# Kernel optimization log

Hardware: AMD Instinct MI355X
Metric: run time of the kernel (lower is better)

## Reference

```python
import jax, jax.numpy as jnp
import numpy as np

NEG = -9e15
EPS = 1e-5

def setup_inputs() -> dict:
    key = jax.random.key(0)
    k1, k2, k3, k4 = jax.random.split(key, 4)
    B, S, D = 4, 2048, 1024
    q = jax.random.normal(k1, (B, S, D), dtype=jnp.float32)
    k = jax.random.normal(k2, (B, S, D), dtype=jnp.float32)
    v = jax.random.normal(k3, (B, S, D), dtype=jnp.float32)
    mask = jax.random.randint(k4, (B, S, S), 0, 2, dtype=jnp.int32)
    gamma = jnp.ones((D,), dtype=jnp.float32)
    beta = jnp.zeros((D,), dtype=jnp.float32)
    return {"q": q, "k": k, "v": v, "mask": mask, "gamma": gamma, "beta": beta}

def reference(q, k, v, mask, gamma, beta):
    d_k = q.shape[-1]
    # scaled dot-product attention: [B,S,S] logits materialized as in original
    logits = jnp.einsum('bsd,btd->bst', q, k) / jnp.sqrt(jnp.asarray(d_k, q.dtype))
    logits = jnp.where(mask == 0, jnp.asarray(NEG, logits.dtype), logits)
    attn = jax.nn.softmax(logits, axis=-1)
    x = jnp.einsum('bst,btd->bsd', attn, v)
    # dropout is identity at inference; LayerNorm over last dim
    mu = jnp.mean(x, axis=-1, keepdims=True)
    var = jnp.mean(jnp.square(x - mu), axis=-1, keepdims=True)
    xhat = (x - mu) * jax.lax.rsqrt(var + EPS)
    return xhat * gamma + beta
```

## Files before the change

### kernel.cpp

```cpp
#include <hip/hip_runtime.h>
#include <hip/hip_bf16.h>

typedef unsigned short u16;
typedef __attribute__((ext_vector_type(8))) short bf16x8;
typedef __attribute__((ext_vector_type(4))) float f32x4;
typedef __attribute__((ext_vector_type(4))) float float4v;
typedef __attribute__((ext_vector_type(4))) short short4v;

#define BB 4
#define SS 2048
#define DD 1024
#define SCALE 0.03125f

__device__ __forceinline__ u16 f2bf(float x){
    unsigned u = __float_as_uint(x);
    return (u16)((u + 0x7fffu + ((u >> 16) & 1u)) >> 16);
}

#define GLD16(g, l) __builtin_amdgcn_global_load_lds( \
    (const __attribute__((address_space(1))) unsigned int*)(g), \
    (__attribute__((address_space(3))) unsigned int*)(l), 16, 0, 0)

__global__ void conv_bf16_kernel(const float* __restrict__ in,
                                 u16* __restrict__ out, int n4){
    int i = blockIdx.x * 256 + threadIdx.x;
    if (i >= n4) return;
    float4v v = ((const float4v*)in)[i];
    short4v o;
    o[0] = (short)f2bf(v[0]); o[1] = (short)f2bf(v[1]);
    o[2] = (short)f2bf(v[2]); o[3] = (short)f2bf(v[3]);
    ((short4v*)out)[i] = o;
}

__global__ void transpose_v_kernel(const float* __restrict__ v,
                                   u16* __restrict__ vt){
    __shared__ float tile[64][65];
    const int b  = blockIdx.z;
    const int s0 = blockIdx.x << 6;
    const int d0 = blockIdx.y << 6;
    const int tx = threadIdx.x & 15;
    const int ty = threadIdx.x >> 4;
#pragma unroll
    for (int kk = 0; kk < 4; ++kk){
        const float* p = v + ((b * SS + s0 + ty + 16 * kk) * DD) + d0 + tx * 4;
        float4v val = *(const float4v*)p;
        tile[ty + 16 * kk][tx * 4 + 0] = val[0];
        tile[ty + 16 * kk][tx * 4 + 1] = val[1];
        tile[ty + 16 * kk][tx * 4 + 2] = val[2];
        tile[ty + 16 * kk][tx * 4 + 3] = val[3];
    }
    __syncthreads();
#pragma unroll
    for (int kk = 0; kk < 4; ++kk){
        int dy = ty + 16 * kk;
        short4v o;
        o[0] = (short)f2bf(tile[tx * 4 + 0][dy]);
        o[1] = (short)f2bf(tile[tx * 4 + 1][dy]);
        o[2] = (short)f2bf(tile[tx * 4 + 2][dy]);
        o[3] = (short)f2bf(tile[tx * 4 + 3][dy]);
        *(short4v*)&vt[((b * DD + d0 + dy) * SS) + s0 + tx * 4] = o;
    }
}

__global__ void zero_f32(float* __restrict__ p, int n){
    int i = blockIdx.x * 256 + threadIdx.x;
    if (i < n) p[i] = 0.f;
}

__global__ __launch_bounds__(256, 3) void qk_kernel(
    const u16* __restrict__ Qb, const u16* __restrict__ Kb,
    const int* __restrict__ mask, u16* __restrict__ P,
    float* __restrict__ rowsum)
{
    __shared__ __align__(16) u16 Abuf[128 * 32];
    __shared__ __align__(16) u16 Bbuf[128 * 32];
    __shared__ float rsred[2][128];

    const int tid  = threadIdx.x;
    const int wid  = tid >> 6, lane = tid & 63;
    const int l16  = lane & 15, g4 = lane >> 4;
    const int wr   = wid >> 1,  wc = wid & 1;
    const int b    = blockIdx.z;
    const int row0 = blockIdx.x << 7;
    const int col0 = blockIdx.y << 7;

    f32x4 acc[4][4];
    const f32x4 z4 = {0.f, 0.f, 0.f, 0.f};
#pragma unroll
    for (int i = 0; i < 4; ++i)
#pragma unroll
        for (int j = 0; j < 4; ++j) acc[i][j] = z4;

    const int off0 = wid * 1024 + lane * 16;
    const int ar0  = off0 >> 6;
    const int ac0  = (off0 & 63) >> 1;

    const u16* gQ = Qb + ((size_t)(b * SS + row0 + ar0)) * DD + ac0;
    const u16* gK = Kb + ((size_t)(b * SS + col0 + ar0)) * DD + ac0;

    for (int kk = 0; kk < DD; kk += 32){
        GLD16(gQ + kk,           (char*)Abuf + wid * 1024);
        GLD16(gQ + 64 * DD + kk, (char*)Abuf + 4096 + wid * 1024);
        GLD16(gK + kk,           (char*)Bbuf + wid * 1024);
        GLD16(gK + 64 * DD + kk, (char*)Bbuf + 4096 + wid * 1024);
        __syncthreads();
        bf16x8 af[4], bfr[4];
#pragma unroll
        for (int i = 0; i < 4; ++i){
            af[i]  = *(const bf16x8*)&Abuf[(wr * 64 + i * 16 + l16) * 32 + g4 * 8];
            bfr[i] = *(const bf16x8*)&Bbuf[(wc * 64 + i * 16 + l16) * 32 + g4 * 8];
        }
#pragma unroll
        for (int i = 0; i < 4; ++i)
#pragma unroll
            for (int j = 0; j < 4; ++j)
                acc[i][j] = __builtin_amdgcn_mfma_f32_16x16x32_bf16(af[i], bfr[j], acc[i][j], 0, 0, 0);
        __syncthreads();
    }

    float rs[4][4];
#pragma unroll
    for (int i = 0; i < 4; ++i)
#pragma unroll
        for (int r = 0; r < 4; ++r) rs[i][r] = 0.f;

#pragma unroll
    for (int i = 0; i < 4; ++i){
#pragma unroll
        for (int j = 0; j < 4; ++j){
#pragma unroll
            for (int r = 0; r < 4; ++r){
                const int grow = row0 + wr * 64 + i * 16 + g4 * 4 + r;
                const int gcol = col0 + wc * 64 + j * 16 + l16;
                const size_t idx = ((size_t)(b * SS + grow)) * SS + gcol;
                int m = mask[idx];
                float e = m ? __expf(acc[i][j][r] * SCALE) : 0.f;
                P[idx] = f2bf(e);
                rs[i][r] += e;
            }
        }
    }
#pragma unroll
    for (int i = 0; i < 4; ++i)
#pragma unroll
        for (int r = 0; r < 4; ++r){
            float v = rs[i][r];
            v += __shfl_xor(v, 1); v += __shfl_xor(v, 2);
            v += __shfl_xor(v, 4); v += __shfl_xor(v, 8);
            if (l16 == 0) rsred[wc][wr * 64 + i * 16 + g4 * 4 + r] = v;
        }
    __syncthreads();
    if (tid < 128)
        atomicAdd(&rowsum[b * SS + row0 + tid], rsred[0][tid] + rsred[1][tid]);
}

__global__ __launch_bounds__(256, 3) void pv_kernel(
    const u16* __restrict__ P, const u16* __restrict__ Vt,
    const float* __restrict__ rowsum, u16* __restrict__ Xn)
{
    __shared__ __align__(16) u16 Abuf[128 * 32];
    __shared__ __align__(16) u16 Bbuf[128 * 32];

    const int tid  = threadIdx.x;
    const int wid  = tid >> 6, lane = tid & 63;
    const int l16  = lane & 15, g4 = lane >> 4;
    const int wr   = wid >> 1,  wc = wid & 1;
    const int b    = blockIdx.z;
    const int row0 = blockIdx.x << 7;
    const int col0 = blockIdx.y << 7;

    f32x4 acc[4][4];
    const f32x4 z4 = {0.f, 0.f, 0.f, 0.f};
#pragma unroll
    for (int i = 0; i < 4; ++i)
#pragma unroll
        for (int j = 0; j < 4; ++j) acc[i][j] = z4;

    const int off0 = wid * 1024 + lane * 16;
    const int ar0  = off0 >> 6;
    const int ac0  = (off0 & 63) >> 1;

    const u16* gP = P  + ((size_t)(b * SS + row0 + ar0)) * SS + ac0;
    const u16* gV = Vt + ((size_t)(b * DD + col0 + ar0)) * SS + ac0;

    for (int kk = 0; kk < SS; kk += 32){
        GLD16(gP + kk,           (char*)Abuf + wid * 1024);
        GLD16(gP + 64 * SS + kk, (char*)Abuf + 4096 + wid * 1024);
        GLD16(gV + kk,           (char*)Bbuf + wid * 1024);
        GLD16(gV + 64 * SS + kk, (char*)Bbuf + 4096 + wid * 1024);
        __syncthreads();
        bf16x8 af[4], bfr[4];
#pragma unroll
        for (int i = 0; i < 4; ++i){
            af[i]  = *(const bf16x8*)&Abuf[(wr * 64 + i * 16 + l16) * 32 + g4 * 8];
            bfr[i] = *(const bf16x8*)&Bbuf[(wc * 64 + i * 16 + l16) * 32 + g4 * 8];
        }
#pragma unroll
        for (int i = 0; i < 4; ++i)
#pragma unroll
            for (int j = 0; j < 4; ++j)
                acc[i][j] = __builtin_amdgcn_mfma_f32_16x16x32_bf16(af[i], bfr[j], acc[i][j], 0, 0, 0);
        __syncthreads();
    }

#pragma unroll
    for (int i = 0; i < 4; ++i){
        float inv[4];
#pragma unroll
        for (int r = 0; r < 4; ++r)
            inv[r] = 1.f / rowsum[b * SS + row0 + wr * 64 + i * 16 + g4 * 4 + r];
#pragma unroll
        for (int j = 0; j < 4; ++j){
#pragma unroll
            for (int r = 0; r < 4; ++r){
                const int grow = row0 + wr * 64 + i * 16 + g4 * 4 + r;
                const int gcol = col0 + wc * 64 + j * 16 + l16;
                Xn[((size_t)(b * SS + grow)) * DD + gcol] = f2bf(acc[i][j][r] * inv[r]);
            }
        }
    }
}

__global__ __launch_bounds__(256) void ln_kernel(
    const u16* __restrict__ Xn, const float* __restrict__ gamma,
    const float* __restrict__ beta, float* __restrict__ out)
{
    __shared__ float red[2][4];
    const int row = blockIdx.x;
    const int t = threadIdx.x;
    short4v xv = *(const short4v*)&Xn[(size_t)row * DD + t * 4];
    float x[4];
#pragma unroll
    for (int j = 0; j < 4; ++j)
        x[j] = __uint_as_float(((unsigned)(u16)xv[j]) << 16);
    float s  = x[0] + x[1] + x[2] + x[3];
    float sq = x[0]*x[0] + x[1]*x[1] + x[2]*x[2] + x[3]*x[3];
#pragma unroll
    for (int d = 1; d < 64; d <<= 1){ s += __shfl_xor(s, d); sq += __shfl_xor(sq, d); }
    const int wv = t >> 6;
    if ((t & 63) == 0){ red[0][wv] = s; red[1][wv] = sq; }
    __syncthreads();
    float S  = red[0][0] + red[0][1] + red[0][2] + red[0][3];
    float Sq = red[1][0] + red[1][1] + red[1][2] + red[1][3];
    float mu = S * (1.f / 1024.f);
    float var = Sq * (1.f / 1024.f) - mu * mu;
    float rstd = rsqrtf(var + 1e-5f);
    float4v g  = *(const float4v*)&gamma[t * 4];
    float4v be = *(const float4v*)&beta[t * 4];
    float4v o;
#pragma unroll
    for (int j = 0; j < 4; ++j) o[j] = (x[j] - mu) * rstd * g[j] + be[j];
    *(float4v*)&out[(size_t)row * DD + t * 4] = o;
}

extern "C" void kernel_launch(void* const* d_in, const int* in_sizes, int n_in,
                              void* d_out, int out_size, void* d_ws, size_t ws_size,
                              hipStream_t stream) {
    const float* q     = (const float*)d_in[0];
    const float* k     = (const float*)d_in[1];
    const float* v     = (const float*)d_in[2];
    const int*   mask  = (const int*)d_in[3];
    const float* gamma = (const float*)d_in[4];
    const float* beta  = (const float*)d_in[5];
    float* out = (float*)d_out;

    u16* Qb = (u16*)d_ws;
    u16* Kb = Qb + (size_t)BB * SS * DD;
    u16* Vt = Kb + (size_t)BB * SS * DD;
    u16* P  = Vt + (size_t)BB * SS * DD;
    u16* Xn = P  + (size_t)BB * SS * SS;
    float* rowsum = (float*)(Xn + (size_t)BB * SS * DD);

    const int n4 = BB * SS * DD / 4;
    conv_bf16_kernel<<<n4 / 256, 256, 0, stream>>>(q, Qb, n4);
    conv_bf16_kernel<<<n4 / 256, 256, 0, stream>>>(k, Kb, n4);
    transpose_v_kernel<<<dim3(SS / 64, DD / 64, BB), 256, 0, stream>>>(v, Vt);
    zero_f32<<<BB * SS / 256, 256, 0, stream>>>(rowsum, BB * SS);

    qk_kernel<<<dim3(16, 16, BB), 256, 0, stream>>>(Qb, Kb, mask, P, rowsum);
    pv_kernel<<<dim3(16, 8, BB), 256, 0, stream>>>(P, Vt, rowsum, Xn);
    ln_kernel<<<BB * SS, 256, 0, stream>>>(Xn, gamma, beta, out);
}
```

Baseline: 162.9 us.

## Double-buffer LDS tiles in QK and PV GEMMs, swizzle block order, fold scale into Q

Both GEMM kernels now use two LDS buffers, so the global-to-LDS load of the next K-tile is issued before the MFMA work on the current tile, with one barrier per iteration instead of two. The 3D grid becomes a flat grid with an XCD-aware swizzle that groups neighbouring tiles on the same die for better L2 reuse, and the launch-bounds occupancy hint rises from 3 to 4. The 1/sqrt(d) scale moves into the Q bf16 conversion, removing a multiply from the exp epilogue. The risks are higher LDS use per block and a possible shift in bf16 rounding because the scale is now applied before conversion.

```diff
diff --git a/kernel.cpp b/kernel.cpp
--- a/kernel.cpp
+++ b/kernel.cpp
@@ -10,7 +10,6 @@
 #define BB 4
 #define SS 2048
 #define DD 1024
-#define SCALE 0.03125f
 
 __device__ __forceinline__ u16 f2bf(float x){
     unsigned u = __float_as_uint(x);
@@ -22,13 +21,13 @@
     (__attribute__((address_space(3))) unsigned int*)(l), 16, 0, 0)
 
 __global__ void conv_bf16_kernel(const float* __restrict__ in,
-                                 u16* __restrict__ out, int n4){
+                                 u16* __restrict__ out, int n4, float scale){
     int i = blockIdx.x * 256 + threadIdx.x;
     if (i >= n4) return;
     float4v v = ((const float4v*)in)[i];
     short4v o;
-    o[0] = (short)f2bf(v[0]); o[1] = (short)f2bf(v[1]);
-    o[2] = (short)f2bf(v[2]); o[3] = (short)f2bf(v[3]);
+    o[0] = (short)f2bf(v[0] * scale); o[1] = (short)f2bf(v[1] * scale);
+    o[2] = (short)f2bf(v[2] * scale); o[3] = (short)f2bf(v[3] * scale);
     ((short4v*)out)[i] = o;
 }
 
@@ -67,22 +66,25 @@
     if (i < n) p[i] = 0.f;
 }
 
-__global__ __launch_bounds__(256, 3) void qk_kernel(
+__global__ __launch_bounds__(256, 4) void qk_kernel(
     const u16* __restrict__ Qb, const u16* __restrict__ Kb,
     const int* __restrict__ mask, u16* __restrict__ P,
     float* __restrict__ rowsum)
 {
-    __shared__ __align__(16) u16 Abuf[128 * 32];
-    __shared__ __align__(16) u16 Bbuf[128 * 32];
+    __shared__ __align__(16) u16 Abuf[2][128 * 32];
+    __shared__ __align__(16) u16 Bbuf[2][128 * 32];
     __shared__ float rsred[2][128];
+
+    const int flat = blockIdx.x;
+    const int swz  = (flat & 7) * 128 + (flat >> 3);
+    const int bx = swz & 15, by = (swz >> 4) & 15, b = swz >> 8;
 
     const int tid  = threadIdx.x;
     const int wid  = tid >> 6, lane = tid & 63;
     const int l16  = lane & 15, g4 = lane >> 4;
     const int wr   = wid >> 1,  wc = wid & 1;
-    const int b    = blockIdx.z;
-    const int row0 = blockIdx.x << 7;
-    const int col0 = blockIdx.y << 7;
+    const int row0 = bx << 7;
+    const int col0 = by << 7;
 
     f32x4 acc[4][4];
     const f32x4 z4 = {0.f, 0.f, 0.f, 0.f};
@@ -94,21 +96,29 @@
     const int off0 = wid * 1024 + lane * 16;
     const int ar0  = off0 >> 6;
     const int ac0  = (off0 & 63) >> 1;
+    const int ldso = wid * 1024 + lane * 16;
 
     const u16* gQ = Qb + ((size_t)(b * SS + row0 + ar0)) * DD + ac0;
     const u16* gK = Kb + ((size_t)(b * SS + col0 + ar0)) * DD + ac0;
 
-    for (int kk = 0; kk < DD; kk += 32){
-        GLD16(gQ + kk,           (char*)Abuf + wid * 1024);
-        GLD16(gQ + 64 * DD + kk, (char*)Abuf + 4096 + wid * 1024);
-        GLD16(gK + kk,           (char*)Bbuf + wid * 1024);
-        GLD16(gK + 64 * DD + kk, (char*)Bbuf + 4096 + wid * 1024);
-        __syncthreads();
+#define QK_STAGE(t, bi) { \
+    GLD16(gQ + (t) * 32,            (char*)Abuf[bi] + ldso); \
+    GLD16(gQ + 64 * DD + (t) * 32,  (char*)Abuf[bi] + 4096 + ldso); \
+    GLD16(gK + (t) * 32,            (char*)Bbuf[bi] + ldso); \
+    GLD16(gK + 64 * DD + (t) * 32,  (char*)Bbuf[bi] + 4096 + ldso); }
+
+    QK_STAGE(0, 0);
+    __syncthreads();
+
+    const int NT = DD / 32;
+    for (int t = 0; t < NT; ++t){
+        const int cur = t & 1;
+        if (t + 1 < NT) QK_STAGE(t + 1, cur ^ 1);
         bf16x8 af[4], bfr[4];
 #pragma unroll
         for (int i = 0; i < 4; ++i){
-            af[i]  = *(const bf16x8*)&Abuf[(wr * 64 + i * 16 + l16) * 32 + g4 * 8];
-            bfr[i] = *(const bf16x8*)&Bbuf[(wc * 64 + i * 16 + l16) * 32 + g4 * 8];
+            af[i]  = *(const bf16x8*)&Abuf[cur][(wr * 64 + i * 16 + l16) * 32 + g4 * 8];
+            bfr[i] = *(const bf16x8*)&Bbuf[cur][(wc * 64 + i * 16 + l16) * 32 + g4 * 8];
         }
 #pragma unroll
         for (int i = 0; i < 4; ++i)
@@ -117,6 +127,7 @@
                 acc[i][j] = __builtin_amdgcn_mfma_f32_16x16x32_bf16(af[i], bfr[j], acc[i][j], 0, 0, 0);
         __syncthreads();
     }
+#undef QK_STAGE
 
     float rs[4][4];
 #pragma unroll
@@ -134,7 +145,7 @@
                 const int gcol = col0 + wc * 64 + j * 16 + l16;
                 const size_t idx = ((size_t)(b * SS + grow)) * SS + gcol;
                 int m = mask[idx];
-                float e = m ? __expf(acc[i][j][r] * SCALE) : 0.f;
+                float e = m ? __expf(acc[i][j][r]) : 0.f;
                 P[idx] = f2bf(e);
                 rs[i][r] += e;
             }
@@ -154,20 +165,23 @@
         atomicAdd(&rowsum[b * SS + row0 + tid], rsred[0][tid] + rsred[1][tid]);
 }
 
-__global__ __launch_bounds__(256, 3) void pv_kernel(
+__global__ __launch_bounds__(256, 4) void pv_kernel(
     const u16* __restrict__ P, const u16* __restrict__ Vt,
     const float* __restrict__ rowsum, u16* __restrict__ Xn)
 {
-    __shared__ __align__(16) u16 Abuf[128 * 32];
-    __shared__ __align__(16) u16 Bbuf[128 * 32];
+    __shared__ __align__(16) u16 Abuf[2][128 * 32];
+    __shared__ __align__(16) u16 Bbuf[2][128 * 32];
+
+    const int flat = blockIdx.x;
+    const int swz  = (flat & 7) * 64 + (flat >> 3);
+    const int bx = swz & 15, by = (swz >> 4) & 7, b = swz >> 7;
 
     const int tid  = threadIdx.x;
     const int wid  = tid >> 6, lane = tid & 63;
     const int l16  = lane & 15, g4 = lane >> 4;
     const int wr   = wid >> 1,  wc = wid & 1;
-    const int b    = blockIdx.z;
-    const int row0 = blockIdx.x << 7;
-    const int col0 = blockIdx.y << 7;
+    const int row0 = bx << 7;
+    const int col0 = by << 7;
 
     f32x4 acc[4][4];
     const f32x4 z4 = {0.f, 0.f, 0.f, 0.f};
@@ -179,21 +193,29 @@
     const int off0 = wid * 1024 + lane * 16;
     const int ar0  = off0 >> 6;
     const int ac0  = (off0 & 63) >> 1;
+    const int ldso = wid * 1024 + lane * 16;
 
     const u16* gP = P  + ((size_t)(b * SS + row0 + ar0)) * SS + ac0;
     const u16* gV = Vt + ((size_t)(b * DD + col0 + ar0)) * SS + ac0;
 
-    for (int kk = 0; kk < SS; kk += 32){
-        GLD16(gP + kk,           (char*)Abuf + wid * 1024);
-        GLD16(gP + 64 * SS + kk, (char*)Abuf + 4096 + wid * 1024);
-        GLD16(gV + kk,           (char*)Bbuf + wid * 1024);
-        GLD16(gV + 64 * SS + kk, (char*)Bbuf + 4096 + wid * 1024);
-        __syncthreads();
+#define PV_STAGE(t, bi) { \
+    GLD16(gP + (t) * 32,            (char*)Abuf[bi] + ldso); \
+    GLD16(gP + 64 * SS + (t) * 32,  (char*)Abuf[bi] + 4096 + ldso); \
+    GLD16(gV + (t) * 32,            (char*)Bbuf[bi] + ldso); \
+    GLD16(gV + 64 * SS + (t) * 32,  (char*)Bbuf[bi] + 4096 + ldso); }
+
+    PV_STAGE(0, 0);
+    __syncthreads();
+
+    const int NT = SS / 32;
+    for (int t = 0; t < NT; ++t){
+        const int cur = t & 1;
+        if (t + 1 < NT) PV_STAGE(t + 1, cur ^ 1);
         bf16x8 af[4], bfr[4];
 #pragma unroll
         for (int i = 0; i < 4; ++i){
-            af[i]  = *(const bf16x8*)&Abuf[(wr * 64 + i * 16 + l16) * 32 + g4 * 8];
-            bfr[i] = *(const bf16x8*)&Bbuf[(wc * 64 + i * 16 + l16) * 32 + g4 * 8];
+            af[i]  = *(const bf16x8*)&Abuf[cur][(wr * 64 + i * 16 + l16) * 32 + g4 * 8];
+            bfr[i] = *(const bf16x8*)&Bbuf[cur][(wc * 64 + i * 16 + l16) * 32 + g4 * 8];
         }
 #pragma unroll
         for (int i = 0; i < 4; ++i)
@@ -202,6 +224,7 @@
                 acc[i][j] = __builtin_amdgcn_mfma_f32_16x16x32_bf16(af[i], bfr[j], acc[i][j], 0, 0, 0);
         __syncthreads();
     }
+#undef PV_STAGE
 
 #pragma unroll
     for (int i = 0; i < 4; ++i){
@@ -272,12 +295,12 @@
     float* rowsum = (float*)(Xn + (size_t)BB * SS * DD);
 
     const int n4 = BB * SS * DD / 4;
-    conv_bf16_kernel<<<n4 / 256, 256, 0, stream>>>(q, Qb, n4);
-    conv_bf16_kernel<<<n4 / 256, 256, 0, stream>>>(k, Kb, n4);
+    conv_bf16_kernel<<<n4 / 256, 256, 0, stream>>>(q, Qb, n4, 0.03125f);
+    conv_bf16_kernel<<<n4 / 256, 256, 0, stream>>>(k, Kb, n4, 1.0f);
     transpose_v_kernel<<<dim3(SS / 64, DD / 64, BB), 256, 0, stream>>>(v, Vt);
     zero_f32<<<BB * SS / 256, 256, 0, stream>>>(rowsum, BB * SS);
 
-    qk_kernel<<<dim3(16, 16, BB), 256, 0, stream>>>(Qb, Kb, mask, P, rowsum);
-    pv_kernel<<<dim3(16, 8, BB), 256, 0, stream>>>(P, Vt, rowsum, Xn);
+    qk_kernel<<<BB * 16 * 16, 256, 0, stream>>>(Qb, Kb, mask, P, rowsum);
+    pv_kernel<<<BB * 16 * 8, 256, 0, stream>>>(P, Vt, rowsum, Xn);
     ln_kernel<<<BB * SS, 256, 0, stream>>>(Xn, gamma, beta, out);
 }
```

New measurement: 162.7 us. No clear change (-0.2%).

## Rewrite QK and PV GEMMs with larger swizzled tiles and double-buffered pipelining

Applied to the files above, without the earlier changes.

Both matmul kernels move to 512-thread blocks with larger tiles (256x256 for QK, 128x256 for PV) and a BK of 64. Global-to-LDS loads are double-buffered with explicit vmcnt waits, and MFMA phases are wrapped in s_setprio and sched barriers. LDS reads use an XOR-swizzled layout to avoid bank conflicts, and the grid is a 1D launch remapped for locality. The 1/sqrt(d) scale is folded into the Q bf16 conversion, and row sums are now accumulated with per-wave atomics. This costs more LDS and registers per block, lowering occupancy, and adds more atomic traffic on the row sums.

```diff
diff --git a/kernel.cpp b/kernel.cpp
--- a/kernel.cpp
+++ b/kernel.cpp
@@ -10,7 +10,6 @@
 #define BB 4
 #define SS 2048
 #define DD 1024
-#define SCALE 0.03125f
 
 __device__ __forceinline__ u16 f2bf(float x){
     unsigned u = __float_as_uint(x);
@@ -21,14 +20,18 @@
     (const __attribute__((address_space(1))) unsigned int*)(g), \
     (__attribute__((address_space(3))) unsigned int*)(l), 16, 0, 0)
 
+#define SCHED0() __builtin_amdgcn_sched_barrier(0)
+#define PH_PRE()  SCHED0(); __builtin_amdgcn_s_barrier(); SCHED0(); __builtin_amdgcn_s_setprio(1)
+#define PH_POST() __builtin_amdgcn_s_setprio(0); SCHED0(); __builtin_amdgcn_s_barrier(); SCHED0()
+
 __global__ void conv_bf16_kernel(const float* __restrict__ in,
-                                 u16* __restrict__ out, int n4){
+                                 u16* __restrict__ out, int n4, float scale){
     int i = blockIdx.x * 256 + threadIdx.x;
     if (i >= n4) return;
     float4v v = ((const float4v*)in)[i];
     short4v o;
-    o[0] = (short)f2bf(v[0]); o[1] = (short)f2bf(v[1]);
-    o[2] = (short)f2bf(v[2]); o[3] = (short)f2bf(v[3]);
+    o[0] = (short)f2bf(v[0] * scale); o[1] = (short)f2bf(v[1] * scale);
+    o[2] = (short)f2bf(v[2] * scale); o[3] = (short)f2bf(v[3] * scale);
     ((short4v*)out)[i] = o;
 }
 
@@ -67,107 +70,175 @@
     if (i < n) p[i] = 0.f;
 }
 
-__global__ __launch_bounds__(256, 3) void qk_kernel(
+__global__ __launch_bounds__(512, 2) void qk_kernel(
     const u16* __restrict__ Qb, const u16* __restrict__ Kb,
     const int* __restrict__ mask, u16* __restrict__ P,
     float* __restrict__ rowsum)
 {
-    __shared__ __align__(16) u16 Abuf[128 * 32];
-    __shared__ __align__(16) u16 Bbuf[128 * 32];
-    __shared__ float rsred[2][128];
-
-    const int tid  = threadIdx.x;
-    const int wid  = tid >> 6, lane = tid & 63;
-    const int l16  = lane & 15, g4 = lane >> 4;
-    const int wr   = wid >> 1,  wc = wid & 1;
-    const int b    = blockIdx.z;
-    const int row0 = blockIdx.x << 7;
-    const int col0 = blockIdx.y << 7;
-
-    f32x4 acc[4][4];
+    __shared__ __align__(16) u16 As[2][256 * 64];
+    __shared__ __align__(16) u16 Bs[2][256 * 64];
+
+    const int swz = ((blockIdx.x & 7) << 5) + (blockIdx.x >> 3);
+    const int b   = swz >> 6;
+    const int bx  = (swz >> 3) & 7;
+    const int by  = swz & 7;
+    const int row0 = bx << 8, col0 = by << 8;
+
+    const int tid = threadIdx.x;
+    const int wid = tid >> 6, lane = tid & 63;
+    const int l16 = lane & 15, g4 = lane >> 4;
+    const int wr = wid >> 2, wc = wid & 3;
+
+    const int sr   = tid >> 3;
+    const int scol = ((tid & 7) ^ (sr & 7)) << 3;
+    const u16* gA = Qb + (size_t)(b * SS + row0 + sr) * DD + scol;
+    const u16* gB = Kb + (size_t)(b * SS + col0 + sr) * DD + scol;
+    char* const lA0 = (char*)As[0] + tid * 16;
+    char* const lB0 = (char*)Bs[0] + tid * 16;
+    char* const lA1 = (char*)As[1] + tid * 16;
+    char* const lB1 = (char*)Bs[1] + tid * 16;
+
+    const int aRow = (wr * 128 + l16) << 7;
+    const int bRow = (wc * 64  + l16) << 7;
+    const int cx0  = (g4 << 4) ^ ((l16 & 7) << 4);
+
+    f32x4 acc[8][4];
     const f32x4 z4 = {0.f, 0.f, 0.f, 0.f};
 #pragma unroll
-    for (int i = 0; i < 4; ++i)
+    for (int i = 0; i < 8; ++i)
 #pragma unroll
         for (int j = 0; j < 4; ++j) acc[i][j] = z4;
 
-    const int off0 = wid * 1024 + lane * 16;
-    const int ar0  = off0 >> 6;
-    const int ac0  = (off0 & 63) >> 1;
-
-    const u16* gQ = Qb + ((size_t)(b * SS + row0 + ar0)) * DD + ac0;
-    const u16* gK = Kb + ((size_t)(b * SS + col0 + ar0)) * DD + ac0;
-
-    for (int kk = 0; kk < DD; kk += 32){
-        GLD16(gQ + kk,           (char*)Abuf + wid * 1024);
-        GLD16(gQ + 64 * DD + kk, (char*)Abuf + 4096 + wid * 1024);
-        GLD16(gK + kk,           (char*)Bbuf + wid * 1024);
-        GLD16(gK + 64 * DD + kk, (char*)Bbuf + 4096 + wid * 1024);
-        __syncthreads();
-        bf16x8 af[4], bfr[4];
-#pragma unroll
-        for (int i = 0; i < 4; ++i){
-            af[i]  = *(const bf16x8*)&Abuf[(wr * 64 + i * 16 + l16) * 32 + g4 * 8];
-            bfr[i] = *(const bf16x8*)&Bbuf[(wc * 64 + i * 16 + l16) * 32 + g4 * 8];
-        }
-#pragma unroll
-        for (int i = 0; i < 4; ++i)
-#pragma unroll
-            for (int j = 0; j < 4; ++j)
-                acc[i][j] = __builtin_amdgcn_mfma_f32_16x16x32_bf16(af[i], bfr[j], acc[i][j], 0, 0, 0);
-        __syncthreads();
-    }
-
-    float rs[4][4];
-#pragma unroll
-    for (int i = 0; i < 4; ++i)
-#pragma unroll
-        for (int r = 0; r < 4; ++r) rs[i][r] = 0.f;
-
-#pragma unroll
-    for (int i = 0; i < 4; ++i){
-#pragma unroll
-        for (int j = 0; j < 4; ++j){
+#define STAGE_QK(kt, la, lb) { \
+    const u16* ga_ = gA + (kt) * 64; \
+    const u16* gb_ = gB + (kt) * 64; \
+    GLD16(ga_,            (la)); \
+    GLD16(ga_ +  64 * DD, (la) + 8192); \
+    GLD16(ga_ + 128 * DD, (la) + 16384); \
+    GLD16(ga_ + 192 * DD, (la) + 24576); \
+    GLD16(gb_,            (lb)); \
+    GLD16(gb_ +  64 * DD, (lb) + 8192); \
+    GLD16(gb_ + 128 * DD, (lb) + 16384); \
+    GLD16(gb_ + 192 * DD, (lb) + 24576); }
+
+#define LDA4(Ab_, mh, kx) { \
+    const char* p_ = (const char*)(Ab_) + aRow + (mh) * 8192 + ((kx) ? (cx0 ^ 64) : cx0); \
+    fa0 = *(const bf16x8*)(p_); \
+    fa1 = *(const bf16x8*)(p_ + 2048); \
+    fa2 = *(const bf16x8*)(p_ + 4096); \
+    fa3 = *(const bf16x8*)(p_ + 6144); }
+
+#define LDB4(Bb_, kx) { \
+    const char* p_ = (const char*)(Bb_) + bRow + ((kx) ? (cx0 ^ 64) : cx0); \
+    fb0 = *(const bf16x8*)(p_); \
+    fb1 = *(const bf16x8*)(p_ + 2048); \
+    fb2 = *(const bf16x8*)(p_ + 4096); \
+    fb3 = *(const bf16x8*)(p_ + 6144); }
+
+#define MROWQ(mi, fa) \
+    acc[mi][0] = __builtin_amdgcn_mfma_f32_16x16x32_bf16(fa, fb0, acc[mi][0],0,0,0); \
+    acc[mi][1] = __builtin_amdgcn_mfma_f32_16x16x32_bf16(fa, fb1, acc[mi][1],0,0,0); \
+    acc[mi][2] = __builtin_amdgcn_mfma_f32_16x16x32_bf16(fa, fb2, acc[mi][2],0,0,0); \
+    acc[mi][3] = __builtin_amdgcn_mfma_f32_16x16x32_bf16(fa, fb3, acc[mi][3],0,0,0);
+
+    STAGE_QK(0, lA0, lB0);
+    STAGE_QK(1, lA1, lB1);
+    asm volatile("s_waitcnt vmcnt(8)" ::: "memory");
+    SCHED0(); __builtin_amdgcn_s_barrier(); SCHED0();
+
+#pragma unroll 1
+    for (int it = 0; it < 8; ++it){
+        bf16x8 fa0, fa1, fa2, fa3, fb0, fb1, fb2, fb3;
+        LDA4(As[0], 0, 0); LDB4(Bs[0], 0);
+        PH_PRE(); MROWQ(0,fa0) MROWQ(1,fa1) MROWQ(2,fa2) MROWQ(3,fa3) PH_POST();
+        LDA4(As[0], 1, 0);
+        PH_PRE(); MROWQ(4,fa0) MROWQ(5,fa1) MROWQ(6,fa2) MROWQ(7,fa3) PH_POST();
+        LDA4(As[0], 0, 1); LDB4(Bs[0], 1);
+        PH_PRE(); MROWQ(0,fa0) MROWQ(1,fa1) MROWQ(2,fa2) MROWQ(3,fa3) PH_POST();
+        LDA4(As[0], 1, 1);
+        PH_PRE(); MROWQ(4,fa0) MROWQ(5,fa1) MROWQ(6,fa2) MROWQ(7,fa3) PH_POST();
+        if (it < 7){
+            STAGE_QK(2*it+2, lA0, lB0);
+            asm volatile("s_waitcnt vmcnt(8)" ::: "memory");
+        } else {
+            asm volatile("s_waitcnt vmcnt(0)" ::: "memory");
+        }
+        SCHED0(); __builtin_amdgcn_s_barrier(); SCHED0();
+        LDA4(As[1], 0, 0); LDB4(Bs[1], 0);
+        PH_PRE(); MROWQ(0,fa0) MROWQ(1,fa1) MROWQ(2,fa2) MROWQ(3,fa3) PH_POST();
+        LDA4(As[1], 1, 0);
+        PH_PRE(); MROWQ(4,fa0) MROWQ(5,fa1) MROWQ(6,fa2) MROWQ(7,fa3) PH_POST();
+        LDA4(As[1], 0, 1); LDB4(Bs[1], 1);
+        PH_PRE(); MROWQ(0,fa0) MROWQ(1,fa1) MROWQ(2,fa2) MROWQ(3,fa3) PH_POST();
+        LDA4(As[1], 1, 1);
+        PH_PRE(); MROWQ(4,fa0) MROWQ(5,fa1) MROWQ(6,fa2) MROWQ(7,fa3) PH_POST();
+        if (it < 7){
+            STAGE_QK(2*it+3, lA1, lB1);
+            asm volatile("s_waitcnt vmcnt(8)" ::: "memory");
+            SCHED0(); __builtin_amdgcn_s_barrier(); SCHED0();
+        }
+    }
+#undef STAGE_QK
+#undef LDA4
+#undef LDB4
+#undef MROWQ
+
+#pragma unroll
+    for (int m = 0; m < 8; ++m){
+        float rsum[4] = {0.f, 0.f, 0.f, 0.f};
+#pragma unroll
+        for (int n = 0; n < 4; ++n){
+            const int gcol = col0 + wc * 64 + n * 16 + l16;
 #pragma unroll
             for (int r = 0; r < 4; ++r){
-                const int grow = row0 + wr * 64 + i * 16 + g4 * 4 + r;
-                const int gcol = col0 + wc * 64 + j * 16 + l16;
-                const size_t idx = ((size_t)(b * SS + grow)) * SS + gcol;
-                int m = mask[idx];
-                float e = m ? __expf(acc[i][j][r] * SCALE) : 0.f;
+                const int grow = row0 + wr * 128 + m * 16 + g4 * 4 + r;
+                const size_t idx = (size_t)(b * SS + grow) * SS + gcol;
+                float e = mask[idx] ? __expf(acc[m][n][r]) : 0.f;
                 P[idx] = f2bf(e);
-                rs[i][r] += e;
+                rsum[r] += e;
             }
         }
-    }
-#pragma unroll
-    for (int i = 0; i < 4; ++i)
 #pragma unroll
         for (int r = 0; r < 4; ++r){
-            float v = rs[i][r];
-            v += __shfl_xor(v, 1); v += __shfl_xor(v, 2);
-            v += __shfl_xor(v, 4); v += __shfl_xor(v, 8);
-            if (l16 == 0) rsred[wc][wr * 64 + i * 16 + g4 * 4 + r] = v;
-        }
-    __syncthreads();
-    if (tid < 128)
-        atomicAdd(&rowsum[b * SS + row0 + tid], rsred[0][tid] + rsred[1][tid]);
-}
-
-__global__ __launch_bounds__(256, 3) void pv_kernel(
+            float v2 = rsum[r];
+            v2 += __shfl_xor(v2, 1); v2 += __shfl_xor(v2, 2);
+            v2 += __shfl_xor(v2, 4); v2 += __shfl_xor(v2, 8);
+            if (l16 == 0)
+                atomicAdd(&rowsum[b * SS + row0 + wr * 128 + m * 16 + g4 * 4 + r], v2);
+        }
+    }
+}
+
+__global__ __launch_bounds__(512, 2) void pv_kernel(
     const u16* __restrict__ P, const u16* __restrict__ Vt,
     const float* __restrict__ rowsum, u16* __restrict__ Xn)
 {
-    __shared__ __align__(16) u16 Abuf[128 * 32];
-    __shared__ __align__(16) u16 Bbuf[128 * 32];
-
-    const int tid  = threadIdx.x;
-    const int wid  = tid >> 6, lane = tid & 63;
-    const int l16  = lane & 15, g4 = lane >> 4;
-    const int wr   = wid >> 1,  wc = wid & 1;
-    const int b    = blockIdx.z;
-    const int row0 = blockIdx.x << 7;
-    const int col0 = blockIdx.y << 7;
+    __shared__ __align__(16) u16 As[2][128 * 64];
+    __shared__ __align__(16) u16 Bs[2][256 * 64];
+
+    const int swz = ((blockIdx.x & 7) << 5) + (blockIdx.x >> 3);
+    const int b   = swz >> 6;
+    const int bx  = (swz >> 2) & 15;
+    const int by  = swz & 3;
+    const int row0 = bx << 7, col0 = by << 8;
+
+    const int tid = threadIdx.x;
+    const int wid = tid >> 6, lane = tid & 63;
+    const int l16 = lane & 15, g4 = lane >> 4;
+    const int wr = wid >> 2, wc = wid & 3;
+
+    const int sr   = tid >> 3;
+    const int scol = ((tid & 7) ^ (sr & 7)) << 3;
+    const u16* gA = P  + (size_t)(b * SS + row0 + sr) * SS + scol;
+    const u16* gB = Vt + (size_t)(b * DD + col0 + sr) * SS + scol;
+    char* const lA0 = (char*)As[0] + tid * 16;
+    char* const lB0 = (char*)Bs[0] + tid * 16;
+    char* const lA1 = (char*)As[1] + tid * 16;
+    char* const lB1 = (char*)Bs[1] + tid * 16;
+
+    const int aRow = (wr * 64 + l16) << 7;
+    const int bRow = (wc * 64 + l16) << 7;
+    const int cx0  = (g4 << 4) ^ ((l16 & 7) << 4);
 
     f32x4 acc[4][4];
     const f32x4 z4 = {0.f, 0.f, 0.f, 0.f};
@@ -176,46 +247,89 @@
 #pragma unroll
         for (int j = 0; j < 4; ++j) acc[i][j] = z4;
 
-    const int off0 = wid * 1024 + lane * 16;
-    const int ar0  = off0 >> 6;
-    const int ac0  = (off0 & 63) >> 1;
-
-    const u16* gP = P  + ((size_t)(b * SS + row0 + ar0)) * SS + ac0;
-    const u16* gV = Vt + ((size_t)(b * DD + col0 + ar0)) * SS + ac0;
-
-    for (int kk = 0; kk < SS; kk += 32){
-        GLD16(gP + kk,           (char*)Abuf + wid * 1024);
-        GLD16(gP + 64 * SS + kk, (char*)Abuf + 4096 + wid * 1024);
-        GLD16(gV + kk,           (char*)Bbuf + wid * 1024);
-        GLD16(gV + 64 * SS + kk, (char*)Bbuf + 4096 + wid * 1024);
-        __syncthreads();
-        bf16x8 af[4], bfr[4];
-#pragma unroll
-        for (int i = 0; i < 4; ++i){
-            af[i]  = *(const bf16x8*)&Abuf[(wr * 64 + i * 16 + l16) * 32 + g4 * 8];
-            bfr[i] = *(const bf16x8*)&Bbuf[(wc * 64 + i * 16 + l16) * 32 + g4 * 8];
-        }
-#pragma unroll
-        for (int i = 0; i < 4; ++i)
-#pragma unroll
-            for (int j = 0; j < 4; ++j)
-                acc[i][j] = __builtin_amdgcn_mfma_f32_16x16x32_bf16(af[i], bfr[j], acc[i][j], 0, 0, 0);
-        __syncthreads();
-    }
-
-#pragma unroll
-    for (int i = 0; i < 4; ++i){
+#define STAGE_PV(kt, la, lb) { \
+    const u16* ga_ = gA + (kt) * 64; \
+    const u16* gb_ = gB + (kt) * 64; \
+    GLD16(ga_,            (la)); \
+    GLD16(ga_ +  64 * SS, (la) + 8192); \
+    GLD16(gb_,            (lb)); \
+    GLD16(gb_ +  64 * SS, (lb) + 8192); \
+    GLD16(gb_ + 128 * SS, (lb) + 16384); \
+    GLD16(gb_ + 192 * SS, (lb) + 24576); }
+
+#define LDA2(Ab_, mh, kx) { \
+    const char* p_ = (const char*)(Ab_) + aRow + (mh) * 4096 + ((kx) ? (cx0 ^ 64) : cx0); \
+    fa0 = *(const bf16x8*)(p_); \
+    fa1 = *(const bf16x8*)(p_ + 2048); }
+
+#define LDB4(Bb_, kx) { \
+    const char* p_ = (const char*)(Bb_) + bRow + ((kx) ? (cx0 ^ 64) : cx0); \
+    fb0 = *(const bf16x8*)(p_); \
+    fb1 = *(const bf16x8*)(p_ + 2048); \
+    fb2 = *(const bf16x8*)(p_ + 4096); \
+    fb3 = *(const bf16x8*)(p_ + 6144); }
+
+#define MROWP(mi, fa) \
+    acc[mi][0] = __builtin_amdgcn_mfma_f32_16x16x32_bf16(fa, fb0, acc[mi][0],0,0,0); \
+    acc[mi][1] = __builtin_amdgcn_mfma_f32_16x16x32_bf16(fa, fb1, acc[mi][1],0,0,0); \
+    acc[mi][2] = __builtin_amdgcn_mfma_f32_16x16x32_bf16(fa, fb2, acc[mi][2],0,0,0); \
+    acc[mi][3] = __builtin_amdgcn_mfma_f32_16x16x32_bf16(fa, fb3, acc[mi][3],0,0,0);
+
+    STAGE_PV(0, lA0, lB0);
+    STAGE_PV(1, lA1, lB1);
+    asm volatile("s_waitcnt vmcnt(6)" ::: "memory");
+    SCHED0(); __builtin_amdgcn_s_barrier(); SCHED0();
+
+#pragma unroll 1
+    for (int it = 0; it < 16; ++it){
+        bf16x8 fa0, fa1, fb0, fb1, fb2, fb3;
+        LDA2(As[0], 0, 0); LDB4(Bs[0], 0);
+        PH_PRE(); MROWP(0,fa0) MROWP(1,fa1) PH_POST();
+        LDA2(As[0], 1, 0);
+        PH_PRE(); MROWP(2,fa0) MROWP(3,fa1) PH_POST();
+        LDA2(As[0], 0, 1); LDB4(Bs[0], 1);
+        PH_PRE(); MROWP(0,fa0) MROWP(1,fa1) PH_POST();
+        LDA2(As[0], 1, 1);
+        PH_PRE(); MROWP(2,fa0) MROWP(3,fa1) PH_POST();
+        if (it < 15){
+            STAGE_PV(2*it+2, lA0, lB0);
+            asm volatile("s_waitcnt vmcnt(6)" ::: "memory");
+        } else {
+            asm volatile("s_waitcnt vmcnt(0)" ::: "memory");
+        }
+        SCHED0(); __builtin_amdgcn_s_barrier(); SCHED0();
+        LDA2(As[1], 0, 0); LDB4(Bs[1], 0);
+        PH_PRE(); MROWP(0,fa0) MROWP(1,fa1) PH_POST();
+        LDA2(As[1], 1, 0);
+        PH_PRE(); MROWP(2,fa0) MROWP(3,fa1) PH_POST();
+        LDA2(As[1], 0, 1); LDB4(Bs[1], 1);
+        PH_PRE(); MROWP(0,fa0) MROWP(1,fa1) PH_POST();
+        LDA2(As[1], 1, 1);
+        PH_PRE(); MROWP(2,fa0) MROWP(3,fa1) PH_POST();
+        if (it < 15){
+            STAGE_PV(2*it+3, lA1, lB1);
+            asm volatile("s_waitcnt vmcnt(6)" ::: "memory");
+            SCHED0(); __builtin_amdgcn_s_barrier(); SCHED0();
+        }
+    }
+#undef STAGE_PV
+#undef LDA2
+#undef LDB4
+#undef MROWP
+
+#pragma unroll
+    for (int m = 0; m < 4; ++m){
         float inv[4];
 #pragma unroll
         for (int r = 0; r < 4; ++r)
-            inv[r] = 1.f / rowsum[b * SS + row0 + wr * 64 + i * 16 + g4 * 4 + r];
-#pragma unroll
-        for (int j = 0; j < 4; ++j){
+            inv[r] = 1.f / rowsum[b * SS + row0 + wr * 64 + m * 16 + g4 * 4 + r];
+#pragma unroll
+        for (int n = 0; n < 4; ++n){
+            const int gcol = col0 + wc * 64 + n * 16 + l16;
 #pragma unroll
             for (int r = 0; r < 4; ++r){
-                const int grow = row0 + wr * 64 + i * 16 + g4 * 4 + r;
-                const int gcol = col0 + wc * 64 + j * 16 + l16;
-                Xn[((size_t)(b * SS + grow)) * DD + gcol] = f2bf(acc[i][j][r] * inv[r]);
+                const int grow = row0 + wr * 64 + m * 16 + g4 * 4 + r;
+                Xn[(size_t)(b * SS + grow) * DD + gcol] = f2bf(acc[m][n][r] * inv[r]);
             }
         }
     }
@@ -272,12 +386,12 @@
     float* rowsum = (float*)(Xn + (size_t)BB * SS * DD);
 
     const int n4 = BB * SS * DD / 4;
-    conv_bf16_kernel<<<n4 / 256, 256, 0, stream>>>(q, Qb, n4);
-    conv_bf16_kernel<<<n4 / 256, 256, 0, stream>>>(k, Kb, n4);
+    conv_bf16_kernel<<<n4 / 256, 256, 0, stream>>>(q, Qb, n4, 0.03125f);
+    conv_bf16_kernel<<<n4 / 256, 256, 0, stream>>>(k, Kb, n4, 1.0f);
     transpose_v_kernel<<<dim3(SS / 64, DD / 64, BB), 256, 0, stream>>>(v, Vt);
     zero_f32<<<BB * SS / 256, 256, 0, stream>>>(rowsum, BB * SS);
 
-    qk_kernel<<<dim3(16, 16, BB), 256, 0, stream>>>(Qb, Kb, mask, P, rowsum);
-    pv_kernel<<<dim3(16, 8, BB), 256, 0, stream>>>(P, Vt, rowsum, Xn);
+    qk_kernel<<<256, 512, 0, stream>>>(Qb, Kb, mask, P, rowsum);
+    pv_kernel<<<256, 512, 0, stream>>>(P, Vt, rowsum, Xn);
     ln_kernel<<<BB * SS, 256, 0, stream>>>(Xn, gamma, beta, out);
 }
```

Result: faster. 145.1 us (-11.0%).
